# Kernel optimization log

Hardware: AMD Instinct MI355X
Metric: run time of the kernel (lower is better)

## Reference

```python
import jax, jax.numpy as jnp
import numpy as np

B, T, S, D, H, HD, DFF, NB = 2, 2048, 2048, 768, 12, 64, 3072, 32
HID = H * HD
EPS = 1e-6
NEG = -1e9


def rmsnorm(x, w):
    # T5 RMSNorm: no mean subtraction, no bias
    var = jnp.mean(jnp.square(x), axis=-1, keepdims=True)
    return x * jax.lax.rsqrt(var + EPS) * w


def sdpa(h, kv, m, wq, wk, wv, wo):
    # h: [B,Tq,D], kv: [B,Tk,D], m: additive mask broadcastable to [B,H,Tq,Tk]
    b, tq, _ = h.shape
    tk = kv.shape[1]
    q = (h @ wq).reshape(b, tq, H, HD)
    k = (kv @ wk).reshape(b, tk, H, HD)
    v = (kv @ wv).reshape(b, tk, H, HD)
    scores = jnp.einsum('bthd,bshd->bhts', q, k) + m  # scale=1.0 (T5)
    p = jax.nn.softmax(scores, axis=-1)
    y = jnp.einsum('bhts,bshd->bthd', p, v).reshape(b, tq, HID)
    return y @ wo


def setup_inputs() -> dict:
    key = jax.random.key(0)
    ks = jax.random.split(key, 16)
    x = jax.random.normal(ks[0], (B, T, D), dtype=jnp.float32)
    # causal additive mask for decoder self-attention
    causal = jnp.tril(jnp.ones((T, T), dtype=bool))
    mask = jnp.broadcast_to(jnp.where(causal, 0.0, NEG)[None, None], (B, 1, T, T)).astype(jnp.float32)
    relative_position = jax.random.randint(ks[1], (1, 1, T, T), 0, NB)
    encoder_hidden_states = jax.random.normal(ks[2], (B, S, D), dtype=jnp.float32)
    encoder_attention_mask = jnp.zeros((B, 1, T, S), dtype=jnp.float32)
    sc = 0.02
    p = {
        'sn_w': jnp.ones((D,), jnp.float32),
        'wq': sc * jax.random.normal(ks[3], (D, HID)),
        'wk': sc * jax.random.normal(ks[4], (D, HID)),
        'wv': sc * jax.random.normal(ks[5], (D, HID)),
        'wo': sc * jax.random.normal(ks[6], (HID, D)),
        'rel_emb': sc * jax.random.normal(ks[7], (NB, H)),
        'cn_w': jnp.ones((D,), jnp.float32),
        'cwq': sc * jax.random.normal(ks[8], (D, HID)),
        'cwk': sc * jax.random.normal(ks[9], (D, HID)),
        'cwv': sc * jax.random.normal(ks[10], (D, HID)),
        'cwo': sc * jax.random.normal(ks[11], (HID, D)),
        'pn_w': jnp.ones((D,), jnp.float32),
        'ffn_wi': sc * jax.random.normal(ks[12], (D, DFF)),
        'ffn_wo': sc * jax.random.normal(ks[13], (DFF, D)),
    }
    return dict(x=x, mask=mask, relative_position=relative_position,
                encoder_hidden_states=encoder_hidden_states,
                encoder_attention_mask=encoder_attention_mask, **p)


def reference(x, mask, relative_position, encoder_hidden_states, encoder_attention_mask,
              sn_w, wq, wk, wv, wo, rel_emb, cn_w, cwq, cwk, cwv, cwo, pn_w, ffn_wi, ffn_wo):
    # self-attention with relative-position bias added into additive mask
    h = rmsnorm(x, sn_w)
    # rel_emb[relative_position]: [1,1,T,T,H] -> permute(0,1,4,2,3) -> squeeze(0) -> [1,H,T,T]
    position_bias = jnp.transpose(rel_emb[relative_position], (0, 1, 4, 2, 3))[0]
    self_mask = mask + position_bias
    y = sdpa(h, h, self_mask, wq, wk, wv, wo)
    attn_out = y + x
    # cross-attention (no relative bias -> zeros position bias)
    enc_dec_position_bias = jnp.zeros_like(encoder_attention_mask)
    h2 = rmsnorm(attn_out, cn_w)
    y2 = sdpa(h2, encoder_hidden_states, encoder_attention_mask + enc_dec_position_bias,
              cwq, cwk, cwv, cwo)
    attn_out = y2 + attn_out
    # T5 FFN: relu(x @ wi) @ wo, pre-norm, residual
    hn = rmsnorm(attn_out, pn_w)
    ff = jax.nn.relu(hn @ ffn_wi) @ ffn_wo
    return (attn_out + ff, position_bias, enc_dec_position_bias)
```

## Files before the change

kernel.cpp:

```cpp
#include <hip/hip_runtime.h>
#include <hip/hip_bf16.h>
#include <stdint.h>

#define T5_B   2
#define T5_T   2048
#define T5_S   2048
#define T5_D   768
#define T5_H   12
#define T5_HD  64
#define T5_DFF 3072
#define T5_NB  32
#define NROW   4096

typedef __attribute__((ext_vector_type(8))) short bf16x8;
typedef __attribute__((ext_vector_type(4))) short short4v;
typedef __attribute__((ext_vector_type(4))) float f32x4;

__device__ __forceinline__ unsigned short f2bf(float x) {
  unsigned int u = __float_as_uint(x);
  unsigned int r = (u + 0x7FFFu + ((u >> 16) & 1u)) >> 16;
  return (unsigned short)r;
}

__device__ __forceinline__ void load_lds16(const void* g, void* l) {
  __builtin_amdgcn_global_load_lds(
      (__attribute__((address_space(1))) void*)(const_cast<void*>(g)),
      (__attribute__((address_space(3))) void*)(l), 16, 0, 0);
}

__device__ __forceinline__ unsigned cvt_pk_bf16(float lo_, float hi_) {
  unsigned d;
  asm("v_cvt_pk_bf16_f32 %0, %1, %2" : "=v"(d) : "v"(lo_), "v"(hi_));
  return d;
}

__device__ __forceinline__ f32x4 mfma16(short4v a, short4v b, f32x4 c) {
#if __has_builtin(__builtin_amdgcn_mfma_f32_16x16x16bf16_1k)
  return __builtin_amdgcn_mfma_f32_16x16x16bf16_1k(a, b, c, 0, 0, 0);
#else
  asm volatile("v_mfma_f32_16x16x16_bf16 %0, %1, %2, %0" : "+v"(c) : "v"(a), "v"(b));
  return c;
#endif
}

struct PrepArgs {
  const float* wsrc[10];
  unsigned short* wdst[10];
  const float* enc; unsigned short* encb;
  const int* rp; unsigned char* rp8;
};

__global__ __launch_bounds__(256)
void prep_kernel(PrepArgs a) {
  __shared__ float tile[32][33];
  const int bid = blockIdx.x, tid = threadIdx.x;
  if (bid < 9216) {
    int widx, rem, Kd, Nd;
    if (bid < 4608)      { widx = bid / 576; rem = bid % 576;  Kd = 768;  Nd = 768;  }
    else if (bid < 6912) { widx = 8;         rem = bid - 4608; Kd = 768;  Nd = 3072; }
    else                 { widx = 9;         rem = bid - 6912; Kd = 3072; Nd = 768;  }
    const float* W = a.wsrc[widx];
    unsigned short* Wt = a.wdst[widx];
    int nb = Nd / 32;
    int n0 = (rem % nb) * 32, k0 = (rem / nb) * 32;
    int tx = tid & 31, ty = tid >> 5;
#pragma unroll
    for (int i = 0; i < 32; i += 8)
      tile[ty + i][tx] = W[(size_t)(k0 + ty + i) * Nd + n0 + tx];
    __syncthreads();
#pragma unroll
    for (int i = 0; i < 32; i += 8)
      Wt[(size_t)(n0 + ty + i) * Kd + k0 + tx] = f2bf(tile[tx][ty + i]);
  } else if (bid < 12288) {
    int i = (bid - 9216) * 256 + tid;
    float4 v = ((const float4*)a.enc)[i];
    unsigned long long pk = (unsigned long long)f2bf(v.x)
                          | ((unsigned long long)f2bf(v.y) << 16)
                          | ((unsigned long long)f2bf(v.z) << 32)
                          | ((unsigned long long)f2bf(v.w) << 48);
    *(unsigned long long*)(a.encb + (size_t)i * 4) = pk;
  } else {
    int idx = (bid - 12288) * 256 + tid;
    const int4* src = (const int4*)(a.rp + (size_t)idx * 16);
    int4 v0 = src[0], v1 = src[1], v2 = src[2], v3 = src[3];
    uint4 o;
    o.x = (v0.x & 31) | ((v0.y & 31) << 8) | ((v0.z & 31) << 16) | ((v0.w & 31) << 24);
    o.y = (v1.x & 31) | ((v1.y & 31) << 8) | ((v1.z & 31) << 16) | ((v1.w & 31) << 24);
    o.z = (v2.x & 31) | ((v2.y & 31) << 8) | ((v2.z & 31) << 16) | ((v2.w & 31) << 24);
    o.w = (v3.x & 31) | ((v3.y & 31) << 8) | ((v3.z & 31) << 16) | ((v3.w & 31) << 24);
    ((uint4*)a.rp8)[idx] = o;
  }
}

__global__ __launch_bounds__(256)
void rmsnorm_kernel(const float* __restrict__ in, const float* __restrict__ w,
                    unsigned short* __restrict__ out) {
  int row = blockIdx.x, tid = threadIdx.x;
  const float* r = in + (size_t)row * 768;
  float x0 = r[tid], x1 = r[tid + 256], x2 = r[tid + 512];
  float s = x0 * x0 + x1 * x1 + x2 * x2;
#pragma unroll
  for (int off = 32; off > 0; off >>= 1) s += __shfl_xor(s, off);
  __shared__ float ws_[4];
  int lane = tid & 63, wv = tid >> 6;
  if (lane == 0) ws_[wv] = s;
  __syncthreads();
  float tot = ws_[0] + ws_[1] + ws_[2] + ws_[3];
  float rinv = rsqrtf(tot * (1.0f / 768.0f) + 1e-6f);
  unsigned short* o = out + (size_t)row * 768;
  o[tid]       = f2bf(x0 * rinv * w[tid]);
  o[tid + 256] = f2bf(x1 * rinv * w[tid + 256]);
  o[tid + 512] = f2bf(x2 * rinv * w[tid + 512]);
}

__global__ __launch_bounds__(256)
void pos_bias_kernel(const int* __restrict__ rp, const float* __restrict__ rel_emb,
                     float* __restrict__ out1, float* __restrict__ out2) {
  __shared__ float rl[384];
  int tid = threadIdx.x;
  for (int i = tid; i < 384; i += 256) rl[i] = rel_emb[i];
  __syncthreads();
  int t = blockIdx.y;
  int s = blockIdx.x * 1024 + tid * 4;
  int4 nb = *(const int4*)(rp + (size_t)t * 2048 + s);
#pragma unroll
  for (int h = 0; h < 12; ++h) {
    float4 v = make_float4(rl[nb.x * 12 + h], rl[nb.y * 12 + h],
                           rl[nb.z * 12 + h], rl[nb.w * 12 + h]);
    *(float4*)(out1 + ((size_t)h * 2048 + t) * 2048 + s) = v;
  }
  size_t base = (((size_t)blockIdx.y * 2 + blockIdx.x) * 256 + tid) * 8;
  float4 z = make_float4(0.f, 0.f, 0.f, 0.f);
  *(float4*)(out2 + base)     = z;
  *(float4*)(out2 + base + 4) = z;
}

__global__ __launch_bounds__(256)
void transpose_v_kernel(const unsigned short* __restrict__ vin, int stride,
                        unsigned short* __restrict__ vT) {
  __shared__ __align__(16) unsigned short tile[64][72];
  int t0 = blockIdx.x * 64, h = blockIdx.y, b = blockIdx.z;
  int tid = threadIdx.x;
  {
    int tl = tid >> 2, d0 = (tid & 3) * 16;
    const unsigned short* src = vin + (size_t)(b * 2048 + t0 + tl) * stride + h * 64 + d0;
    *(bf16x8*)&tile[tl][d0]     = *(const bf16x8*)src;
    *(bf16x8*)&tile[tl][d0 + 8] = *(const bf16x8*)(src + 8);
  }
  __syncthreads();
  {
    int d = tid >> 2, t1 = (tid & 3) * 16;
    unsigned short tmp[16] __attribute__((aligned(16)));
#pragma unroll
    for (int j = 0; j < 16; ++j) tmp[j] = tile[t1 + j][d];
    unsigned short* dst = vT + ((size_t)((b * 12 + h) * 64 + d)) * 2048 + t0 + t1;
    *(bf16x8*)dst       = *(bf16x8*)&tmp[0];
    *(bf16x8*)(dst + 8) = *(bf16x8*)&tmp[8];
  }
}

template <int TM, int TN, int EPI>
__global__ __launch_bounds__(256)
void gemm_bt(const unsigned short* __restrict__ A, const unsigned short* __restrict__ Bt,
             void* __restrict__ C, const float* __restrict__ res, int N, int K) {
  constexpr int WR = (TM >= 128) ? 2 : 1;
  constexpr int WC = 4 / WR;
  constexpr int AM = TM / WR / 16;
  constexpr int AN = TN / WC / 16;
  constexpr int CHA = TM / 8, CHB = TN / 8, CPW = (CHA + CHB) / 4;
  __shared__ __align__(16) unsigned short Als[2][TM * 64];
  __shared__ __align__(16) unsigned short Bls[2][TN * 64];
  const int tid = threadIdx.x, lane = tid & 63, wv = tid >> 6;
  const int lo = lane & 15, hi = lane >> 4;
  const int wr = wv / WC, wc = wv % WC;

  int gx = gridDim.x;
  int nwg = gx * gridDim.y;
  int f = blockIdx.y * gx + blockIdx.x;
  int q8 = nwg >> 3, r8 = nwg & 7, xcd = f & 7, base = f >> 3;
  int wg = (xcd < r8 ? xcd * (q8 + 1) : r8 * (q8 + 1) + (xcd - r8) * q8) + base;
  const int m0 = (wg / gx) * TM, n0 = (wg % gx) * TN;

  f32x4 acc[AM][AN];
#pragma unroll
  for (int i = 0; i < AM; ++i)
#pragma unroll
    for (int j = 0; j < AN; ++j) acc[i][j] = f32x4{0.f, 0.f, 0.f, 0.f};

  const int srr  = lane >> 3;
  const int scol = ((lane & 7) ^ srr) * 8;

  auto stage = [&](int k0, int bsel) {
#pragma unroll
    for (int j = 0; j < CPW; ++j) {
      int c = wv * CPW + j;
      if (c < CHA)
        load_lds16(A + (size_t)(m0 + c * 8 + srr) * K + k0 + scol, &Als[bsel][c * 512]);
      else {
        int c2 = c - CHA;
        load_lds16(Bt + (size_t)(n0 + c2 * 8 + srr) * K + k0 + scol, &Bls[bsel][c2 * 512]);
      }
    }
  };

  stage(0, 0);
  const int nIt = K >> 6;
  for (int it = 0; it < nIt; ++it) {
    const int bsel = it & 1;
    if (it + 1 < nIt) {
      stage((it + 1) << 6, bsel ^ 1);
      asm volatile("s_waitcnt vmcnt(%0)" :: "n"(CPW) : "memory");
    } else {
      asm volatile("s_waitcnt vmcnt(0)" ::: "memory");
    }
    __builtin_amdgcn_s_barrier();
    __builtin_amdgcn_sched_barrier(0);
#pragma unroll
    for (int kk = 0; kk < 2; ++kk) {
      bf16x8 af[AM], bfr[AN];
#pragma unroll
      for (int i = 0; i < AM; ++i) {
        int row = wr * (AM * 16) + i * 16 + lo;
        unsigned by = (unsigned)(row * 128) + ((unsigned)(((kk * 4 + hi) ^ (row & 7))) << 4);
        af[i] = *(const bf16x8*)((const char*)&Als[bsel][0] + by);
      }
#pragma unroll
      for (int j = 0; j < AN; ++j) {
        int row = wc * (AN * 16) + j * 16 + lo;
        unsigned by = (unsigned)(row * 128) + ((unsigned)(((kk * 4 + hi) ^ (row & 7))) << 4);
        bfr[j] = *(const bf16x8*)((const char*)&Bls[bsel][0] + by);
      }
      __builtin_amdgcn_s_setprio(1);
#pragma unroll
      for (int i = 0; i < AM; ++i)
#pragma unroll
        for (int j = 0; j < AN; ++j)
          acc[i][j] = __builtin_amdgcn_mfma_f32_16x16x32_bf16(af[i], bfr[j], acc[i][j], 0, 0, 0);
      __builtin_amdgcn_s_setprio(0);
    }
    __builtin_amdgcn_sched_barrier(0);
    __builtin_amdgcn_s_barrier();
  }

#pragma unroll
  for (int mi = 0; mi < AM; ++mi)
#pragma unroll
    for (int ni = 0; ni < AN; ++ni) {
      int row = m0 + wr * (AM * 16) + mi * 16 + hi * 4;
      int col = n0 + wc * (AN * 16) + ni * 16 + lo;
#pragma unroll
      for (int r = 0; r < 4; ++r) {
        float v = acc[mi][ni][r];
        size_t idx = (size_t)(row + r) * N + col;
        if (EPI == 0) {
          ((unsigned short*)C)[idx] = f2bf(v);
        } else if (EPI == 1) {
          ((float*)C)[idx] = v + res[idx];
        } else {
          ((unsigned short*)C)[idx] = f2bf(fmaxf(v, 0.0f));
        }
      }
    }
}

template <bool SELF>
__global__ __launch_bounds__(256)
void attn_kernel(const unsigned short* __restrict__ qp, int qstride,
                 const unsigned short* __restrict__ kp, int kstride,
                 const unsigned short* __restrict__ vT,
                 const unsigned char* __restrict__ rp8, const float* __restrict__ rel_emb,
                 unsigned short* __restrict__ yp) {
  __shared__ __align__(16) unsigned short Kls[2][4096];
  __shared__ __align__(16) unsigned short Vls[2][4096];
  __shared__ __align__(16) unsigned char rp8t[SELF ? 2 * 8192 : 16];
  __shared__ float rel_l[32];

  const int tid = threadIdx.x, lane = tid & 63, wv = tid >> 6;
  const int lo = lane & 15, hi = lane >> 4;
  const int h = blockIdx.y, b = blockIdx.z;
  const int qta = SELF ? (int)blockIdx.x : (int)blockIdx.x * 2;
  const int qtb = SELF ? 31 - (int)blockIdx.x : (int)blockIdx.x * 2 + 1;
  const int ntiles = SELF ? qtb + 1 : 32;

  if (SELF && tid < 32) rel_l[tid] = rel_emb[tid * 12 + h];

  const int qA = qta * 64 + wv * 16 + lo;
  const int qB = qtb * 64 + wv * 16 + lo;
  const unsigned short* qrA = qp + (size_t)(b * T5_T + qA) * qstride + h * 64 + hi * 8;
  const unsigned short* qrB = qp + (size_t)(b * T5_T + qB) * qstride + h * 64 + hi * 8;
  const bf16x8 qa0 = *(const bf16x8*)qrA;
  const bf16x8 qa1 = *(const bf16x8*)(qrA + 32);
  const bf16x8 qb0 = *(const bf16x8*)qrB;
  const bf16x8 qb1 = *(const bf16x8*)(qrB + 32);

  f32x4 OA[4], OB[4];
  float mA = -3.0e38f, lA = 0.f, mB = -3.0e38f, lB = 0.f;
#pragma unroll
  for (int i = 0; i < 4; ++i) { OA[i] = f32x4{0.f, 0.f, 0.f, 0.f}; OB[i] = f32x4{0.f, 0.f, 0.f, 0.f}; }

  const int krr = lane >> 3;
  const int kd0 = ((lane & 7) ^ krr) * 8;

  auto stage = [&](int kt, int bsel) {
    const int s0 = kt * 64;
#pragma unroll
    for (int j = 0; j < 2; ++j) {
      int c = wv * 2 + j;
      int rr = c * 8 + krr;
      load_lds16(kp + (size_t)(b * 2048 + s0 + rr) * kstride + h * 64 + kd0, &Kls[bsel][c * 512]);
      load_lds16(vT + (size_t)((b * 12 + h) * 64 + rr) * 2048 + s0 + kd0,    &Vls[bsel][c * 512]);
    }
    if (SELF) {
      load_lds16(rp8 + (size_t)(qtb * 64 + wv * 16 + (lane >> 2)) * 2048 + s0 + (lane & 3) * 16,
                 &rp8t[bsel * 8192 + 4096 + wv * 1024]);
      if (kt <= qta)
        load_lds16(rp8 + (size_t)(qta * 64 + wv * 16 + (lane >> 2)) * 2048 + s0 + (lane & 3) * 16,
                   &rp8t[bsel * 8192 + wv * 1024]);
    }
  };

  auto qcomp = [&](const bf16x8& qf0, const bf16x8& qf1, f32x4* Oc, float& m_, float& l_,
                   const unsigned char* rt, int qrow, bool edge, int s0,
                   const unsigned short* Kb, const unsigned short* Vb) {
    f32x4 S[4];
    __builtin_amdgcn_s_setprio(1);
#pragma unroll
    for (int ct = 0; ct < 4; ++ct) {
      int krow = ct * 16 + lo;
      unsigned by0 = ((unsigned)(krow * 128 + hi * 16))      ^ ((unsigned)(krow & 7) << 4);
      unsigned by1 = ((unsigned)(krow * 128 + 64 + hi * 16)) ^ ((unsigned)(krow & 7) << 4);
      bf16x8 kf0 = *(const bf16x8*)((const char*)Kb + by0);
      bf16x8 kf1 = *(const bf16x8*)((const char*)Kb + by1);
      f32x4 sa = f32x4{0.f, 0.f, 0.f, 0.f};
      sa = __builtin_amdgcn_mfma_f32_16x16x32_bf16(kf0, qf0, sa, 0, 0, 0);
      sa = __builtin_amdgcn_mfma_f32_16x16x32_bf16(kf1, qf1, sa, 0, 0, 0);
      S[ct] = sa;
    }
    __builtin_amdgcn_s_setprio(0);

    if (SELF) {
#pragma unroll
      for (int ct = 0; ct < 4; ++ct) {
        unsigned nb4 = *(const unsigned*)&rt[lo * 64 + ct * 16 + hi * 4];
#pragma unroll
        for (int r = 0; r < 4; ++r) {
          int s = s0 + ct * 16 + hi * 4 + r;
          float sc = S[ct][r] + rel_l[(nb4 >> (8 * r)) & 31u];
          if (edge && s > qrow) sc = -1e30f;
          S[ct][r] = sc;
        }
      }
    }

    float tm = S[0][0];
#pragma unroll
    for (int ct = 0; ct < 4; ++ct)
#pragma unroll
      for (int r = 0; r < 4; ++r) tm = fmaxf(tm, S[ct][r]);
    tm = fmaxf(tm, __shfl_xor(tm, 16));
    tm = fmaxf(tm, __shfl_xor(tm, 32));
    float mn = fmaxf(m_, tm);
    float alpha = __expf(m_ - mn);
    float rs = 0.f;
#pragma unroll
    for (int ct = 0; ct < 4; ++ct)
#pragma unroll
      for (int r = 0; r < 4; ++r) { float e = __expf(S[ct][r] - mn); S[ct][r] = e; rs += e; }
    rs += __shfl_xor(rs, 16);
    rs += __shfl_xor(rs, 32);
    l_ = l_ * alpha + rs;
    m_ = mn;
#pragma unroll
    for (int dt = 0; dt < 4; ++dt)
#pragma unroll
      for (int r = 0; r < 4; ++r) Oc[dt][r] *= alpha;

    short4v pf[4];
#pragma unroll
    for (int ct = 0; ct < 4; ++ct) {
      union { unsigned u[2]; short4v s; } cv;
      cv.u[0] = cvt_pk_bf16(S[ct][0], S[ct][1]);
      cv.u[1] = cvt_pk_bf16(S[ct][2], S[ct][3]);
      pf[ct] = cv.s;
    }

    __builtin_amdgcn_s_setprio(1);
#pragma unroll
    for (int dt = 0; dt < 4; ++dt) {
      int vrow = dt * 16 + lo;
#pragma unroll
      for (int ct = 0; ct < 4; ++ct) {
        unsigned vb = ((unsigned)(vrow * 128 + ct * 32 + hi * 8)) ^ ((unsigned)(vrow & 7) << 4);
        short4v vf = *(const short4v*)((const char*)Vb + vb);
        Oc[dt] = mfma16(vf, pf[ct], Oc[dt]);
      }
    }
    __builtin_amdgcn_s_setprio(0);
  };

  stage(0, 0);

  for (int kt = 0; kt < ntiles; ++kt) {
    const int bsel = kt & 1;
    const int s0 = kt * 64;
    asm volatile("s_waitcnt vmcnt(0)" ::: "memory");
    __syncthreads();
    if (kt + 1 < ntiles) stage(kt + 1, bsel ^ 1);

    const unsigned short* Kb = &Kls[bsel][0];
    const unsigned short* Vb = &Vls[bsel][0];

    if (!SELF || kt <= qta)
      qcomp(qa0, qa1, OA, mA, lA, &rp8t[bsel * 8192 + wv * 1024], qA,
            SELF && kt == qta, s0, Kb, Vb);
    qcomp(qb0, qb1, OB, mB, lB, &rp8t[bsel * 8192 + 4096 + wv * 1024], qB,
          SELF && kt == qtb, s0, Kb, Vb);
  }

#if !__has_builtin(__builtin_amdgcn_mfma_f32_16x16x16bf16_1k)
  asm volatile("s_nop 7\n\ts_nop 7" ::: );
#endif

  {
    float inv = 1.0f / lA;
    unsigned short* yr = yp + (size_t)(b * T5_T + qA) * 768 + h * 64 + hi * 4;
#pragma unroll
    for (int dt = 0; dt < 4; ++dt) {
      unsigned long long pk = (unsigned long long)f2bf(OA[dt][0] * inv)
                            | ((unsigned long long)f2bf(OA[dt][1] * inv) << 16)
                            | ((unsigned long long)f2bf(OA[dt][2] * inv) << 32)
                            | ((unsigned long long)f2bf(OA[dt][3] * inv) << 48);
      *(unsigned long long*)(yr + dt * 16) = pk;
    }
  }
  {
    float inv = 1.0f / lB;
    unsigned short* yr = yp + (size_t)(b * T5_T + qB) * 768 + h * 64 + hi * 4;
#pragma unroll
    for (int dt = 0; dt < 4; ++dt) {
      unsigned long long pk = (unsigned long long)f2bf(OB[dt][0] * inv)
                            | ((unsigned long long)f2bf(OB[dt][1] * inv) << 16)
                            | ((unsigned long long)f2bf(OB[dt][2] * inv) << 32)
                            | ((unsigned long long)f2bf(OB[dt][3] * inv) << 48);
      *(unsigned long long*)(yr + dt * 16) = pk;
    }
  }
}

extern "C" void kernel_launch(void* const* d_in, const int* in_sizes, int n_in,
                              void* d_out, int out_size, void* d_ws, size_t ws_size,
                              hipStream_t stream) {
  (void)in_sizes; (void)n_in; (void)out_size; (void)ws_size;
  const float* x    = (const float*)d_in[0];
  const int*   rp   = (const int*)d_in[2];
  const float* enc  = (const float*)d_in[3];
  const float* sn_w = (const float*)d_in[5];
  const float* wq   = (const float*)d_in[6];
  const float* wk   = (const float*)d_in[7];
  const float* wvw  = (const float*)d_in[8];
  const float* wo   = (const float*)d_in[9];
  const float* rel  = (const float*)d_in[10];
  const float* cn_w = (const float*)d_in[11];
  const float* cwq  = (const float*)d_in[12];
  const float* cwk  = (const float*)d_in[13];
  const float* cwv  = (const float*)d_in[14];
  const float* cwo  = (const float*)d_in[15];
  const float* pn_w = (const float*)d_in[16];
  const float* wi   = (const float*)d_in[17];
  const float* wo2  = (const float*)d_in[18];

  float* out0 = (float*)d_out;
  float* out1 = out0 + (size_t)NROW * T5_D;
  float* out2 = out1 + (size_t)T5_H * T5_T * T5_T;

  char* ws = (char*)d_ws;
  size_t off = 0;
  auto alloc = [&](size_t bytes) { char* p = ws + off; off += (bytes + 255) & ~(size_t)255; return p; };
  unsigned short* wqkvT = (unsigned short*)alloc((size_t)2304 * 768 * 2);
  unsigned short* woT   = (unsigned short*)alloc((size_t)768 * 768 * 2);
  unsigned short* wckvT = (unsigned short*)alloc((size_t)1536 * 768 * 2);
  unsigned short* wcqT  = (unsigned short*)alloc((size_t)768 * 768 * 2);
  unsigned short* wcoT  = (unsigned short*)alloc((size_t)768 * 768 * 2);
  unsigned short* wiT   = (unsigned short*)alloc((size_t)3072 * 768 * 2);
  unsigned short* woT2  = (unsigned short*)alloc((size_t)768 * 3072 * 2);
  unsigned short* normb = (unsigned short*)alloc((size_t)NROW * 768 * 2);
  unsigned short* encb  = (unsigned short*)alloc((size_t)NROW * 768 * 2);
  unsigned short* ybuf  = (unsigned short*)alloc((size_t)NROW * 768 * 2);
  float*          attn  = (float*)alloc((size_t)NROW * 768 * 4);
  unsigned char*  rp8p  = (unsigned char*)alloc((size_t)2048 * 2048);
  unsigned short* big   = (unsigned short*)alloc((size_t)NROW * 3072 * 2);
  unsigned short* vT    = big + (size_t)NROW * 2304;

  dim3 blk(256);

  {
    PrepArgs pa;
    pa.wsrc[0] = wq;  pa.wdst[0] = wqkvT;
    pa.wsrc[1] = wk;  pa.wdst[1] = wqkvT + 768 * 768;
    pa.wsrc[2] = wvw; pa.wdst[2] = wqkvT + 2 * 768 * 768;
    pa.wsrc[3] = wo;  pa.wdst[3] = woT;
    pa.wsrc[4] = cwk; pa.wdst[4] = wckvT;
    pa.wsrc[5] = cwv; pa.wdst[5] = wckvT + 768 * 768;
    pa.wsrc[6] = cwq; pa.wdst[6] = wcqT;
    pa.wsrc[7] = cwo; pa.wdst[7] = wcoT;
    pa.wsrc[8] = wi;  pa.wdst[8] = wiT;
    pa.wsrc[9] = wo2; pa.wdst[9] = woT2;
    pa.enc = enc; pa.encb = encb; pa.rp = rp; pa.rp8 = rp8p;
    prep_kernel<<<13312, blk, 0, stream>>>(pa);
  }

  rmsnorm_kernel<<<NROW, blk, 0, stream>>>(x, sn_w, normb);

  gemm_bt<128, 128, 0><<<dim3(18, 32), blk, 0, stream>>>(normb, wqkvT, big, nullptr, 2304, 768);
  transpose_v_kernel<<<dim3(32, 12, 2), blk, 0, stream>>>(big + 1536, 2304, vT);
  attn_kernel<true><<<dim3(16, 12, 2), blk, 0, stream>>>(big, 2304, big + 768, 2304, vT, rp8p, rel, ybuf);
  gemm_bt<64, 128, 1><<<dim3(6, 64), blk, 0, stream>>>(ybuf, woT, attn, x, 768, 768);

  pos_bias_kernel<<<dim3(2, 2048), blk, 0, stream>>>(rp, rel, out1, out2);

  rmsnorm_kernel<<<NROW, blk, 0, stream>>>(attn, cn_w, normb);
  gemm_bt<128, 128, 0><<<dim3(12, 32), blk, 0, stream>>>(encb, wckvT, big + (size_t)NROW * 768, nullptr, 1536, 768);
  gemm_bt<64, 128, 0><<<dim3(6, 64), blk, 0, stream>>>(normb, wcqT, big, nullptr, 768, 768);
  transpose_v_kernel<<<dim3(32, 12, 2), blk, 0, stream>>>(big + (size_t)NROW * 768 + 768, 1536, vT);
  attn_kernel<false><<<dim3(16, 12, 2), blk, 0, stream>>>(big, 768, big + (size_t)NROW * 768, 1536, vT,
                                                          nullptr, nullptr, ybuf);
  gemm_bt<64, 128, 1><<<dim3(6, 64), blk, 0, stream>>>(ybuf, wcoT, attn, attn, 768, 768);

  rmsnorm_kernel<<<NROW, blk, 0, stream>>>(attn, pn_w, normb);
  gemm_bt<128, 128, 2><<<dim3(24, 32), blk, 0, stream>>>(normb, wiT, big, nullptr, 3072, 768);
  gemm_bt<64, 128, 1><<<dim3(6, 64), blk, 0, stream>>>(big, woT2, out0, attn, 768, 3072);
}
```

Measured before the change: 386.9 us.

## Merge independent launches into fused stage kernels and split attention kernels

Folds the first RMSNorm into the prep kernel. A new stage1 kernel runs the self-QKV GEMM, the cross-KV GEMM and the position-bias output writes in a single launch, and both V transposes now share one launch. Attention is split into dedicated self and cross kernels, with smaller 64-row query tiles and XCD swizzling on the cross path. Output-projection GEMMs move to 64x64 tiles for more workgroups. The aim is fewer launches and better CU fill, at the cost of mixing heterogeneous work in one grid and extra workspace buffers.

```diff
diff --git a/kernel.cpp b/kernel.cpp
--- a/kernel.cpp
+++ b/kernel.cpp
@@ -43,16 +43,135 @@
 #endif
 }
 
+__device__ __forceinline__ int xcd_swz(int f, int nwg) {
+  int q8 = nwg >> 3, r8 = nwg & 7, xcd = f & 7, base = f >> 3;
+  return (xcd < r8 ? xcd * (q8 + 1) : r8 * (q8 + 1) + (xcd - r8) * q8) + base;
+}
+
+template <int TM, int TN, int EPI>
+__device__ __forceinline__ void gemm_body(
+    int f, int gx, int nwg,
+    const unsigned short* __restrict__ A, const unsigned short* __restrict__ Bt,
+    void* __restrict__ C, const float* __restrict__ res, int N, int K,
+    unsigned short* LDS) {
+  constexpr int WR = (TM >= 128) ? 2 : 1;
+  constexpr int WC = 4 / WR;
+  constexpr int AM = TM / WR / 16;
+  constexpr int AN = TN / WC / 16;
+  constexpr int CHA = TM / 8, CHB = TN / 8, CPW = (CHA + CHB) / 4;
+  constexpr int BUFSH = (TM + TN) * 64;
+  const int tid = threadIdx.x, lane = tid & 63, wv = tid >> 6;
+  const int lo = lane & 15, hi = lane >> 4;
+  const int wr = wv / WC, wc = wv % WC;
+  const int wg = xcd_swz(f, nwg);
+  const int m0 = (wg / gx) * TM, n0 = (wg % gx) * TN;
+
+  f32x4 acc[AM][AN];
+#pragma unroll
+  for (int i = 0; i < AM; ++i)
+#pragma unroll
+    for (int j = 0; j < AN; ++j) acc[i][j] = f32x4{0.f, 0.f, 0.f, 0.f};
+
+  const int srr  = lane >> 3;
+  const int scol = ((lane & 7) ^ srr) * 8;
+
+  auto stage = [&](int k0, int bsel) {
+    unsigned short* Ab = LDS + bsel * BUFSH;
+    unsigned short* Bb = Ab + TM * 64;
+#pragma unroll
+    for (int j = 0; j < CPW; ++j) {
+      int c = wv * CPW + j;
+      if (c < CHA)
+        load_lds16(A + (size_t)(m0 + c * 8 + srr) * K + k0 + scol, Ab + c * 512);
+      else {
+        int c2 = c - CHA;
+        load_lds16(Bt + (size_t)(n0 + c2 * 8 + srr) * K + k0 + scol, Bb + c2 * 512);
+      }
+    }
+  };
+
+  stage(0, 0);
+  const int nIt = K >> 6;
+  for (int it = 0; it < nIt; ++it) {
+    const int bsel = it & 1;
+    if (it + 1 < nIt) {
+      stage((it + 1) << 6, bsel ^ 1);
+      asm volatile("s_waitcnt vmcnt(%0)" :: "n"(CPW) : "memory");
+    } else {
+      asm volatile("s_waitcnt vmcnt(0)" ::: "memory");
+    }
+    __builtin_amdgcn_s_barrier();
+    __builtin_amdgcn_sched_barrier(0);
+    const unsigned short* Ab = LDS + bsel * BUFSH;
+    const unsigned short* Bb = Ab + TM * 64;
+#pragma unroll
+    for (int kk = 0; kk < 2; ++kk) {
+      bf16x8 af[AM], bfr[AN];
+#pragma unroll
+      for (int i = 0; i < AM; ++i) {
+        int row = wr * (AM * 16) + i * 16 + lo;
+        unsigned by = (unsigned)(row * 128) + ((unsigned)(((kk * 4 + hi) ^ (row & 7))) << 4);
+        af[i] = *(const bf16x8*)((const char*)Ab + by);
+      }
+#pragma unroll
+      for (int j = 0; j < AN; ++j) {
+        int row = wc * (AN * 16) + j * 16 + lo;
+        unsigned by = (unsigned)(row * 128) + ((unsigned)(((kk * 4 + hi) ^ (row & 7))) << 4);
+        bfr[j] = *(const bf16x8*)((const char*)Bb + by);
+      }
+      __builtin_amdgcn_s_setprio(1);
+#pragma unroll
+      for (int i = 0; i < AM; ++i)
+#pragma unroll
+        for (int j = 0; j < AN; ++j)
+          acc[i][j] = __builtin_amdgcn_mfma_f32_16x16x32_bf16(af[i], bfr[j], acc[i][j], 0, 0, 0);
+      __builtin_amdgcn_s_setprio(0);
+    }
+    __builtin_amdgcn_sched_barrier(0);
+    __builtin_amdgcn_s_barrier();
+  }
+
+#pragma unroll
+  for (int mi = 0; mi < AM; ++mi)
+#pragma unroll
+    for (int ni = 0; ni < AN; ++ni) {
+      int row = m0 + wr * (AM * 16) + mi * 16 + hi * 4;
+      int col = n0 + wc * (AN * 16) + ni * 16 + lo;
+#pragma unroll
+      for (int r = 0; r < 4; ++r) {
+        float v = acc[mi][ni][r];
+        size_t idx = (size_t)(row + r) * N + col;
+        if (EPI == 0) {
+          ((unsigned short*)C)[idx] = f2bf(v);
+        } else if (EPI == 1) {
+          ((float*)C)[idx] = v + res[idx];
+        } else {
+          ((unsigned short*)C)[idx] = f2bf(fmaxf(v, 0.0f));
+        }
+      }
+    }
+}
+
+template <int TM, int TN, int EPI>
+__global__ __launch_bounds__(256)
+void gemm_bt(const unsigned short* __restrict__ A, const unsigned short* __restrict__ Bt,
+             void* __restrict__ C, const float* __restrict__ res, int N, int K) {
+  __shared__ __align__(16) unsigned short LDS[2 * (TM + TN) * 64];
+  int f = blockIdx.y * gridDim.x + blockIdx.x;
+  gemm_body<TM, TN, EPI>(f, gridDim.x, gridDim.x * gridDim.y, A, Bt, C, res, N, K, LDS);
+}
+
 struct PrepArgs {
   const float* wsrc[10];
   unsigned short* wdst[10];
   const float* enc; unsigned short* encb;
   const int* rp; unsigned char* rp8;
+  const float* x; const float* snw; unsigned short* normb;
 };
 
 __global__ __launch_bounds__(256)
 void prep_kernel(PrepArgs a) {
-  __shared__ float tile[32][33];
+  __shared__ __align__(16) float tile[32][33];
   const int bid = blockIdx.x, tid = threadIdx.x;
   if (bid < 9216) {
     int widx, rem, Kd, Nd;
@@ -79,7 +198,7 @@
                           | ((unsigned long long)f2bf(v.z) << 32)
                           | ((unsigned long long)f2bf(v.w) << 48);
     *(unsigned long long*)(a.encb + (size_t)i * 4) = pk;
-  } else {
+  } else if (bid < 13312) {
     int idx = (bid - 12288) * 256 + tid;
     const int4* src = (const int4*)(a.rp + (size_t)idx * 16);
     int4 v0 = src[0], v1 = src[1], v2 = src[2], v3 = src[3];
@@ -89,6 +208,23 @@
     o.z = (v2.x & 31) | ((v2.y & 31) << 8) | ((v2.z & 31) << 16) | ((v2.w & 31) << 24);
     o.w = (v3.x & 31) | ((v3.y & 31) << 8) | ((v3.z & 31) << 16) | ((v3.w & 31) << 24);
     ((uint4*)a.rp8)[idx] = o;
+  } else {
+    int row = bid - 13312;
+    const float* r = a.x + (size_t)row * 768;
+    float x0 = r[tid], x1 = r[tid + 256], x2 = r[tid + 512];
+    float s = x0 * x0 + x1 * x1 + x2 * x2;
+#pragma unroll
+    for (int off = 32; off > 0; off >>= 1) s += __shfl_xor(s, off);
+    float* wsm = &tile[0][0];
+    int lane = tid & 63, wvv = tid >> 6;
+    if (lane == 0) wsm[wvv] = s;
+    __syncthreads();
+    float tot = wsm[0] + wsm[1] + wsm[2] + wsm[3];
+    float rinv = rsqrtf(tot * (1.0f / 768.0f) + 1e-6f);
+    unsigned short* o = a.normb + (size_t)row * 768;
+    o[tid]       = f2bf(x0 * rinv * a.snw[tid]);
+    o[tid + 256] = f2bf(x1 * rinv * a.snw[tid + 256]);
+    o[tid + 512] = f2bf(x2 * rinv * a.snw[tid + 512]);
   }
 }
 
@@ -113,33 +249,53 @@
   o[tid + 512] = f2bf(x2 * rinv * w[tid + 512]);
 }
 
+struct Stage1Args {
+  const unsigned short *normb, *wqkvT, *encb, *wckvT;
+  unsigned short *qkv, *ckv;
+  const int* rp; const float* rel;
+  float *out1, *out2;
+};
+
 __global__ __launch_bounds__(256)
-void pos_bias_kernel(const int* __restrict__ rp, const float* __restrict__ rel_emb,
-                     float* __restrict__ out1, float* __restrict__ out2) {
-  __shared__ float rl[384];
-  int tid = threadIdx.x;
-  for (int i = tid; i < 384; i += 256) rl[i] = rel_emb[i];
-  __syncthreads();
-  int t = blockIdx.y;
-  int s = blockIdx.x * 1024 + tid * 4;
-  int4 nb = *(const int4*)(rp + (size_t)t * 2048 + s);
-#pragma unroll
-  for (int h = 0; h < 12; ++h) {
-    float4 v = make_float4(rl[nb.x * 12 + h], rl[nb.y * 12 + h],
-                           rl[nb.z * 12 + h], rl[nb.w * 12 + h]);
-    *(float4*)(out1 + ((size_t)h * 2048 + t) * 2048 + s) = v;
-  }
-  size_t base = (((size_t)blockIdx.y * 2 + blockIdx.x) * 256 + tid) * 8;
-  float4 z = make_float4(0.f, 0.f, 0.f, 0.f);
-  *(float4*)(out2 + base)     = z;
-  *(float4*)(out2 + base + 4) = z;
+void stage1_kernel(Stage1Args a) {
+  __shared__ __align__(16) unsigned short LDS[32768];
+  const int bid = blockIdx.x, tid = threadIdx.x;
+  if (bid < 576) {
+    gemm_body<128, 128, 0>(bid, 18, 576, a.normb, a.wqkvT, a.qkv, nullptr, 2304, 768, LDS);
+  } else if (bid < 960) {
+    gemm_body<128, 128, 0>(bid - 576, 12, 384, a.encb, a.wckvT, a.ckv, nullptr, 1536, 768, LDS);
+  } else {
+    const int p = bid - 960;
+    float* rl = (float*)LDS;
+    for (int i = tid; i < 384; i += 256) rl[i] = a.rel[i];
+    __syncthreads();
+    int t = p >> 1;
+    int s = (p & 1) * 1024 + tid * 4;
+    int4 nb = *(const int4*)(a.rp + (size_t)t * 2048 + s);
+#pragma unroll
+    for (int h = 0; h < 12; ++h) {
+      float4 v = make_float4(rl[nb.x * 12 + h], rl[nb.y * 12 + h],
+                             rl[nb.z * 12 + h], rl[nb.w * 12 + h]);
+      *(float4*)(a.out1 + ((size_t)h * 2048 + t) * 2048 + s) = v;
+    }
+    size_t zbase = ((size_t)p * 256 + tid) * 8;
+    float4 z = make_float4(0.f, 0.f, 0.f, 0.f);
+    *(float4*)(a.out2 + zbase)     = z;
+    *(float4*)(a.out2 + zbase + 4) = z;
+  }
 }
 
 __global__ __launch_bounds__(256)
-void transpose_v_kernel(const unsigned short* __restrict__ vin, int stride,
-                        unsigned short* __restrict__ vT) {
+void transpose_both_kernel(const unsigned short* __restrict__ v1,
+                           const unsigned short* __restrict__ v2,
+                           unsigned short* __restrict__ vT1,
+                           unsigned short* __restrict__ vT2) {
   __shared__ __align__(16) unsigned short tile[64][72];
-  int t0 = blockIdx.x * 64, h = blockIdx.y, b = blockIdx.z;
+  int which = blockIdx.z >> 1, b = blockIdx.z & 1;
+  const unsigned short* vin = which ? v2 : v1;
+  int stride = which ? 1536 : 2304;
+  unsigned short* vT = which ? vT2 : vT1;
+  int t0 = blockIdx.x * 64, h = blockIdx.y;
   int tid = threadIdx.x;
   {
     int tl = tid >> 2, d0 = (tid & 3) * 16;
@@ -159,135 +315,126 @@
   }
 }
 
-template <int TM, int TN, int EPI>
+template <bool SELF>
+__device__ __forceinline__ void attn_qcomp(
+    const bf16x8& qf0, const bf16x8& qf1, f32x4* Oc, float& m_, float& l_,
+    const unsigned char* rt, const float* rel_l, int qrow, bool edge, int s0,
+    const unsigned short* Kb, const unsigned short* Vb, int lo, int hi) {
+  f32x4 S[4];
+  __builtin_amdgcn_s_setprio(1);
+#pragma unroll
+  for (int ct = 0; ct < 4; ++ct) {
+    int krow = ct * 16 + lo;
+    unsigned by0 = ((unsigned)(krow * 128 + hi * 16))      ^ ((unsigned)(krow & 7) << 4);
+    unsigned by1 = ((unsigned)(krow * 128 + 64 + hi * 16)) ^ ((unsigned)(krow & 7) << 4);
+    bf16x8 kf0 = *(const bf16x8*)((const char*)Kb + by0);
+    bf16x8 kf1 = *(const bf16x8*)((const char*)Kb + by1);
+    f32x4 sa = f32x4{0.f, 0.f, 0.f, 0.f};
+    sa = __builtin_amdgcn_mfma_f32_16x16x32_bf16(kf0, qf0, sa, 0, 0, 0);
+    sa = __builtin_amdgcn_mfma_f32_16x16x32_bf16(kf1, qf1, sa, 0, 0, 0);
+    S[ct] = sa;
+  }
+  __builtin_amdgcn_s_setprio(0);
+
+  if constexpr (SELF) {
+#pragma unroll
+    for (int ct = 0; ct < 4; ++ct) {
+      unsigned nb4 = *(const unsigned*)&rt[lo * 64 + ct * 16 + hi * 4];
+#pragma unroll
+      for (int r = 0; r < 4; ++r) {
+        int s = s0 + ct * 16 + hi * 4 + r;
+        float sc = S[ct][r] + rel_l[(nb4 >> (8 * r)) & 31u];
+        if (edge && s > qrow) sc = -1e30f;
+        S[ct][r] = sc;
+      }
+    }
+  }
+
+  float tm = S[0][0];
+#pragma unroll
+  for (int ct = 0; ct < 4; ++ct)
+#pragma unroll
+    for (int r = 0; r < 4; ++r) tm = fmaxf(tm, S[ct][r]);
+  tm = fmaxf(tm, __shfl_xor(tm, 16));
+  tm = fmaxf(tm, __shfl_xor(tm, 32));
+  float mn = fmaxf(m_, tm);
+  float alpha = __expf(m_ - mn);
+  float rs = 0.f;
+#pragma unroll
+  for (int ct = 0; ct < 4; ++ct)
+#pragma unroll
+    for (int r = 0; r < 4; ++r) { float e = __expf(S[ct][r] - mn); S[ct][r] = e; rs += e; }
+  rs += __shfl_xor(rs, 16);
+  rs += __shfl_xor(rs, 32);
+  l_ = l_ * alpha + rs;
+  if (tm > m_) {
+#pragma unroll
+    for (int dt = 0; dt < 4; ++dt)
+#pragma unroll
+      for (int r = 0; r < 4; ++r) Oc[dt][r] *= alpha;
+  }
+  m_ = mn;
+
+  short4v pf[4];
+#pragma unroll
+  for (int ct = 0; ct < 4; ++ct) {
+    union { unsigned u[2]; short4v s; } cv;
+    cv.u[0] = cvt_pk_bf16(S[ct][0], S[ct][1]);
+    cv.u[1] = cvt_pk_bf16(S[ct][2], S[ct][3]);
+    pf[ct] = cv.s;
+  }
+
+  __builtin_amdgcn_s_setprio(1);
+#pragma unroll
+  for (int dt = 0; dt < 4; ++dt) {
+    int vrow = dt * 16 + lo;
+#pragma unroll
+    for (int ct = 0; ct < 4; ++ct) {
+      unsigned vb = ((unsigned)(vrow * 128 + ct * 32 + hi * 8)) ^ ((unsigned)(vrow & 7) << 4);
+      short4v vf = *(const short4v*)((const char*)Vb + vb);
+      Oc[dt] = mfma16(vf, pf[ct], Oc[dt]);
+    }
+  }
+  __builtin_amdgcn_s_setprio(0);
+}
+
+__device__ __forceinline__ void attn_store(f32x4* Oc, float l_, unsigned short* yr) {
+  float inv = 1.0f / l_;
+#pragma unroll
+  for (int dt = 0; dt < 4; ++dt) {
+    unsigned long long pk = (unsigned long long)f2bf(Oc[dt][0] * inv)
+                          | ((unsigned long long)f2bf(Oc[dt][1] * inv) << 16)
+                          | ((unsigned long long)f2bf(Oc[dt][2] * inv) << 32)
+                          | ((unsigned long long)f2bf(Oc[dt][3] * inv) << 48);
+    *(unsigned long long*)(yr + dt * 16) = pk;
+  }
+}
+
 __global__ __launch_bounds__(256)
-void gemm_bt(const unsigned short* __restrict__ A, const unsigned short* __restrict__ Bt,
-             void* __restrict__ C, const float* __restrict__ res, int N, int K) {
-  constexpr int WR = (TM >= 128) ? 2 : 1;
-  constexpr int WC = 4 / WR;
-  constexpr int AM = TM / WR / 16;
-  constexpr int AN = TN / WC / 16;
-  constexpr int CHA = TM / 8, CHB = TN / 8, CPW = (CHA + CHB) / 4;
-  __shared__ __align__(16) unsigned short Als[2][TM * 64];
-  __shared__ __align__(16) unsigned short Bls[2][TN * 64];
+void attn_self_kernel(const unsigned short* __restrict__ qp,
+                      const unsigned short* __restrict__ kp,
+                      const unsigned short* __restrict__ vT,
+                      const unsigned char* __restrict__ rp8,
+                      const float* __restrict__ rel_emb,
+                      unsigned short* __restrict__ yp) {
+  __shared__ __align__(16) unsigned short Kls[2][4096];
+  __shared__ __align__(16) unsigned short Vls[2][4096];
+  __shared__ __align__(16) unsigned char rp8t[2][8192];
+  __shared__ float rel_l[32];
+
   const int tid = threadIdx.x, lane = tid & 63, wv = tid >> 6;
   const int lo = lane & 15, hi = lane >> 4;
-  const int wr = wv / WC, wc = wv % WC;
-
-  int gx = gridDim.x;
-  int nwg = gx * gridDim.y;
-  int f = blockIdx.y * gx + blockIdx.x;
-  int q8 = nwg >> 3, r8 = nwg & 7, xcd = f & 7, base = f >> 3;
-  int wg = (xcd < r8 ? xcd * (q8 + 1) : r8 * (q8 + 1) + (xcd - r8) * q8) + base;
-  const int m0 = (wg / gx) * TM, n0 = (wg % gx) * TN;
-
-  f32x4 acc[AM][AN];
-#pragma unroll
-  for (int i = 0; i < AM; ++i)
-#pragma unroll
-    for (int j = 0; j < AN; ++j) acc[i][j] = f32x4{0.f, 0.f, 0.f, 0.f};
-
-  const int srr  = lane >> 3;
-  const int scol = ((lane & 7) ^ srr) * 8;
-
-  auto stage = [&](int k0, int bsel) {
-#pragma unroll
-    for (int j = 0; j < CPW; ++j) {
-      int c = wv * CPW + j;
-      if (c < CHA)
-        load_lds16(A + (size_t)(m0 + c * 8 + srr) * K + k0 + scol, &Als[bsel][c * 512]);
-      else {
-        int c2 = c - CHA;
-        load_lds16(Bt + (size_t)(n0 + c2 * 8 + srr) * K + k0 + scol, &Bls[bsel][c2 * 512]);
-      }
-    }
-  };
-
-  stage(0, 0);
-  const int nIt = K >> 6;
-  for (int it = 0; it < nIt; ++it) {
-    const int bsel = it & 1;
-    if (it + 1 < nIt) {
-      stage((it + 1) << 6, bsel ^ 1);
-      asm volatile("s_waitcnt vmcnt(%0)" :: "n"(CPW) : "memory");
-    } else {
-      asm volatile("s_waitcnt vmcnt(0)" ::: "memory");
-    }
-    __builtin_amdgcn_s_barrier();
-    __builtin_amdgcn_sched_barrier(0);
-#pragma unroll
-    for (int kk = 0; kk < 2; ++kk) {
-      bf16x8 af[AM], bfr[AN];
-#pragma unroll
-      for (int i = 0; i < AM; ++i) {
-        int row = wr * (AM * 16) + i * 16 + lo;
-        unsigned by = (unsigned)(row * 128) + ((unsigned)(((kk * 4 + hi) ^ (row & 7))) << 4);
-        af[i] = *(const bf16x8*)((const char*)&Als[bsel][0] + by);
-      }
-#pragma unroll
-      for (int j = 0; j < AN; ++j) {
-        int row = wc * (AN * 16) + j * 16 + lo;
-        unsigned by = (unsigned)(row * 128) + ((unsigned)(((kk * 4 + hi) ^ (row & 7))) << 4);
-        bfr[j] = *(const bf16x8*)((const char*)&Bls[bsel][0] + by);
-      }
-      __builtin_amdgcn_s_setprio(1);
-#pragma unroll
-      for (int i = 0; i < AM; ++i)
-#pragma unroll
-        for (int j = 0; j < AN; ++j)
-          acc[i][j] = __builtin_amdgcn_mfma_f32_16x16x32_bf16(af[i], bfr[j], acc[i][j], 0, 0, 0);
-      __builtin_amdgcn_s_setprio(0);
-    }
-    __builtin_amdgcn_sched_barrier(0);
-    __builtin_amdgcn_s_barrier();
-  }
-
-#pragma unroll
-  for (int mi = 0; mi < AM; ++mi)
-#pragma unroll
-    for (int ni = 0; ni < AN; ++ni) {
-      int row = m0 + wr * (AM * 16) + mi * 16 + hi * 4;
-      int col = n0 + wc * (AN * 16) + ni * 16 + lo;
-#pragma unroll
-      for (int r = 0; r < 4; ++r) {
-        float v = acc[mi][ni][r];
-        size_t idx = (size_t)(row + r) * N + col;
-        if (EPI == 0) {
-          ((unsigned short*)C)[idx] = f2bf(v);
-        } else if (EPI == 1) {
-          ((float*)C)[idx] = v + res[idx];
-        } else {
-          ((unsigned short*)C)[idx] = f2bf(fmaxf(v, 0.0f));
-        }
-      }
-    }
-}
-
-template <bool SELF>
-__global__ __launch_bounds__(256)
-void attn_kernel(const unsigned short* __restrict__ qp, int qstride,
-                 const unsigned short* __restrict__ kp, int kstride,
-                 const unsigned short* __restrict__ vT,
-                 const unsigned char* __restrict__ rp8, const float* __restrict__ rel_emb,
-                 unsigned short* __restrict__ yp) {
-  __shared__ __align__(16) unsigned short Kls[2][4096];
-  __shared__ __align__(16) unsigned short Vls[2][4096];
-  __shared__ __align__(16) unsigned char rp8t[SELF ? 2 * 8192 : 16];
-  __shared__ float rel_l[32];
-
-  const int tid = threadIdx.x, lane = tid & 63, wv = tid >> 6;
-  const int lo = lane & 15, hi = lane >> 4;
-  const int h = blockIdx.y, b = blockIdx.z;
-  const int qta = SELF ? (int)blockIdx.x : (int)blockIdx.x * 2;
-  const int qtb = SELF ? 31 - (int)blockIdx.x : (int)blockIdx.x * 2 + 1;
-  const int ntiles = SELF ? qtb + 1 : 32;
-
-  if (SELF && tid < 32) rel_l[tid] = rel_emb[tid * 12 + h];
+  const int wg = xcd_swz(blockIdx.x + 16 * (blockIdx.y + 12 * blockIdx.z), 384);
+  const int xq = wg & 15, h = (wg >> 4) % 12, b = (wg >> 4) / 12;
+  const int qta = xq, qtb = 31 - xq;
+  const int ntiles = qtb + 1;
+
+  if (tid < 32) rel_l[tid] = rel_emb[tid * 12 + h];
 
   const int qA = qta * 64 + wv * 16 + lo;
   const int qB = qtb * 64 + wv * 16 + lo;
-  const unsigned short* qrA = qp + (size_t)(b * T5_T + qA) * qstride + h * 64 + hi * 8;
-  const unsigned short* qrB = qp + (size_t)(b * T5_T + qB) * qstride + h * 64 + hi * 8;
+  const unsigned short* qrA = qp + (size_t)(b * T5_T + qA) * 2304 + h * 64 + hi * 8;
+  const unsigned short* qrB = qp + (size_t)(b * T5_T + qB) * 2304 + h * 64 + hi * 8;
   const bf16x8 qa0 = *(const bf16x8*)qrA;
   const bf16x8 qa1 = *(const bf16x8*)(qrA + 32);
   const bf16x8 qb0 = *(const bf16x8*)qrB;
@@ -307,95 +454,14 @@
     for (int j = 0; j < 2; ++j) {
       int c = wv * 2 + j;
       int rr = c * 8 + krr;
-      load_lds16(kp + (size_t)(b * 2048 + s0 + rr) * kstride + h * 64 + kd0, &Kls[bsel][c * 512]);
-      load_lds16(vT + (size_t)((b * 12 + h) * 64 + rr) * 2048 + s0 + kd0,    &Vls[bsel][c * 512]);
-    }
-    if (SELF) {
-      load_lds16(rp8 + (size_t)(qtb * 64 + wv * 16 + (lane >> 2)) * 2048 + s0 + (lane & 3) * 16,
-                 &rp8t[bsel * 8192 + 4096 + wv * 1024]);
-      if (kt <= qta)
-        load_lds16(rp8 + (size_t)(qta * 64 + wv * 16 + (lane >> 2)) * 2048 + s0 + (lane & 3) * 16,
-                   &rp8t[bsel * 8192 + wv * 1024]);
-    }
-  };
-
-  auto qcomp = [&](const bf16x8& qf0, const bf16x8& qf1, f32x4* Oc, float& m_, float& l_,
-                   const unsigned char* rt, int qrow, bool edge, int s0,
-                   const unsigned short* Kb, const unsigned short* Vb) {
-    f32x4 S[4];
-    __builtin_amdgcn_s_setprio(1);
-#pragma unroll
-    for (int ct = 0; ct < 4; ++ct) {
-      int krow = ct * 16 + lo;
-      unsigned by0 = ((unsigned)(krow * 128 + hi * 16))      ^ ((unsigned)(krow & 7) << 4);
-      unsigned by1 = ((unsigned)(krow * 128 + 64 + hi * 16)) ^ ((unsigned)(krow & 7) << 4);
-      bf16x8 kf0 = *(const bf16x8*)((const char*)Kb + by0);
-      bf16x8 kf1 = *(const bf16x8*)((const char*)Kb + by1);
-      f32x4 sa = f32x4{0.f, 0.f, 0.f, 0.f};
-      sa = __builtin_amdgcn_mfma_f32_16x16x32_bf16(kf0, qf0, sa, 0, 0, 0);
-      sa = __builtin_amdgcn_mfma_f32_16x16x32_bf16(kf1, qf1, sa, 0, 0, 0);
-      S[ct] = sa;
-    }
-    __builtin_amdgcn_s_setprio(0);
-
-    if (SELF) {
-#pragma unroll
-      for (int ct = 0; ct < 4; ++ct) {
-        unsigned nb4 = *(const unsigned*)&rt[lo * 64 + ct * 16 + hi * 4];
-#pragma unroll
-        for (int r = 0; r < 4; ++r) {
-          int s = s0 + ct * 16 + hi * 4 + r;
-          float sc = S[ct][r] + rel_l[(nb4 >> (8 * r)) & 31u];
-          if (edge && s > qrow) sc = -1e30f;
-          S[ct][r] = sc;
-        }
-      }
-    }
-
-    float tm = S[0][0];
-#pragma unroll
-    for (int ct = 0; ct < 4; ++ct)
-#pragma unroll
-      for (int r = 0; r < 4; ++r) tm = fmaxf(tm, S[ct][r]);
-    tm = fmaxf(tm, __shfl_xor(tm, 16));
-    tm = fmaxf(tm, __shfl_xor(tm, 32));
-    float mn = fmaxf(m_, tm);
-    float alpha = __expf(m_ - mn);
-    float rs = 0.f;
-#pragma unroll
-    for (int ct = 0; ct < 4; ++ct)
-#pragma unroll
-      for (int r = 0; r < 4; ++r) { float e = __expf(S[ct][r] - mn); S[ct][r] = e; rs += e; }
-    rs += __shfl_xor(rs, 16);
-    rs += __shfl_xor(rs, 32);
-    l_ = l_ * alpha + rs;
-    m_ = mn;
-#pragma unroll
-    for (int dt = 0; dt < 4; ++dt)
-#pragma unroll
-      for (int r = 0; r < 4; ++r) Oc[dt][r] *= alpha;
-
-    short4v pf[4];
-#pragma unroll
-    for (int ct = 0; ct < 4; ++ct) {
-      union { unsigned u[2]; short4v s; } cv;
-      cv.u[0] = cvt_pk_bf16(S[ct][0], S[ct][1]);
-      cv.u[1] = cvt_pk_bf16(S[ct][2], S[ct][3]);
-      pf[ct] = cv.s;
-    }
-
-    __builtin_amdgcn_s_setprio(1);
-#pragma unroll
-    for (int dt = 0; dt < 4; ++dt) {
-      int vrow = dt * 16 + lo;
-#pragma unroll
-      for (int ct = 0; ct < 4; ++ct) {
-        unsigned vb = ((unsigned)(vrow * 128 + ct * 32 + hi * 8)) ^ ((unsigned)(vrow & 7) << 4);
-        short4v vf = *(const short4v*)((const char*)Vb + vb);
-        Oc[dt] = mfma16(vf, pf[ct], Oc[dt]);
-      }
-    }
-    __builtin_amdgcn_s_setprio(0);
+      load_lds16(kp + (size_t)(b * 2048 + s0 + rr) * 2304 + h * 64 + kd0, &Kls[bsel][c * 512]);
+      load_lds16(vT + (size_t)((b * 12 + h) * 64 + rr) * 2048 + s0 + kd0,  &Vls[bsel][c * 512]);
+    }
+    load_lds16(rp8 + (size_t)(qtb * 64 + wv * 16 + (lane >> 2)) * 2048 + s0 + (lane & 3) * 16,
+               &rp8t[bsel][4096 + wv * 1024]);
+    if (kt <= qta)
+      load_lds16(rp8 + (size_t)(qta * 64 + wv * 16 + (lane >> 2)) * 2048 + s0 + (lane & 3) * 16,
+                 &rp8t[bsel][wv * 1024]);
   };
 
   stage(0, 0);
@@ -410,41 +476,74 @@
     const unsigned short* Kb = &Kls[bsel][0];
     const unsigned short* Vb = &Vls[bsel][0];
 
-    if (!SELF || kt <= qta)
-      qcomp(qa0, qa1, OA, mA, lA, &rp8t[bsel * 8192 + wv * 1024], qA,
-            SELF && kt == qta, s0, Kb, Vb);
-    qcomp(qb0, qb1, OB, mB, lB, &rp8t[bsel * 8192 + 4096 + wv * 1024], qB,
-          SELF && kt == qtb, s0, Kb, Vb);
+    if (kt <= qta)
+      attn_qcomp<true>(qa0, qa1, OA, mA, lA, &rp8t[bsel][wv * 1024], rel_l, qA,
+                       kt == qta, s0, Kb, Vb, lo, hi);
+    attn_qcomp<true>(qb0, qb1, OB, mB, lB, &rp8t[bsel][4096 + wv * 1024], rel_l, qB,
+                     kt == qtb, s0, Kb, Vb, lo, hi);
   }
 
 #if !__has_builtin(__builtin_amdgcn_mfma_f32_16x16x16bf16_1k)
   asm volatile("s_nop 7\n\ts_nop 7" ::: );
 #endif
 
-  {
-    float inv = 1.0f / lA;
-    unsigned short* yr = yp + (size_t)(b * T5_T + qA) * 768 + h * 64 + hi * 4;
-#pragma unroll
-    for (int dt = 0; dt < 4; ++dt) {
-      unsigned long long pk = (unsigned long long)f2bf(OA[dt][0] * inv)
-                            | ((unsigned long long)f2bf(OA[dt][1] * inv) << 16)
-                            | ((unsigned long long)f2bf(OA[dt][2] * inv) << 32)
-                            | ((unsigned long long)f2bf(OA[dt][3] * inv) << 48);
-      *(unsigned long long*)(yr + dt * 16) = pk;
-    }
-  }
-  {
-    float inv = 1.0f / lB;
-    unsigned short* yr = yp + (size_t)(b * T5_T + qB) * 768 + h * 64 + hi * 4;
-#pragma unroll
-    for (int dt = 0; dt < 4; ++dt) {
-      unsigned long long pk = (unsigned long long)f2bf(OB[dt][0] * inv)
-                            | ((unsigned long long)f2bf(OB[dt][1] * inv) << 16)
-                            | ((unsigned long long)f2bf(OB[dt][2] * inv) << 32)
-                            | ((unsigned long long)f2bf(OB[dt][3] * inv) << 48);
-      *(unsigned long long*)(yr + dt * 16) = pk;
-    }
-  }
+  attn_store(OA, lA, yp + (size_t)(b * T5_T + qA) * 768 + h * 64 + hi * 4);
+  attn_store(OB, lB, yp + (size_t)(b * T5_T + qB) * 768 + h * 64 + hi * 4);
+}
+
+__global__ __launch_bounds__(256)
+void attn_cross_kernel(const unsigned short* __restrict__ qp,
+                       const unsigned short* __restrict__ kp,
+                       const unsigned short* __restrict__ vT,
+                       unsigned short* __restrict__ yp) {
+  __shared__ __align__(16) unsigned short Kls[2][4096];
+  __shared__ __align__(16) unsigned short Vls[2][4096];
+
+  const int tid = threadIdx.x, lane = tid & 63, wv = tid >> 6;
+  const int lo = lane & 15, hi = lane >> 4;
+  const int wg = xcd_swz(blockIdx.x + 32 * (blockIdx.y + 12 * blockIdx.z), 768);
+  const int xq = wg & 31, h = (wg >> 5) % 12, b = (wg >> 5) / 12;
+
+  const int q = xq * 64 + wv * 16 + lo;
+  const unsigned short* qr = qp + (size_t)(b * T5_T + q) * 768 + h * 64 + hi * 8;
+  const bf16x8 qf0 = *(const bf16x8*)qr;
+  const bf16x8 qf1 = *(const bf16x8*)(qr + 32);
+
+  f32x4 Oc[4];
+  float m_ = -3.0e38f, l_ = 0.f;
+#pragma unroll
+  for (int i = 0; i < 4; ++i) Oc[i] = f32x4{0.f, 0.f, 0.f, 0.f};
+
+  const int krr = lane >> 3;
+  const int kd0 = ((lane & 7) ^ krr) * 8;
+
+  auto stage = [&](int kt, int bsel) {
+    const int s0 = kt * 64;
+#pragma unroll
+    for (int j = 0; j < 2; ++j) {
+      int c = wv * 2 + j;
+      int rr = c * 8 + krr;
+      load_lds16(kp + (size_t)(b * 2048 + s0 + rr) * 1536 + h * 64 + kd0, &Kls[bsel][c * 512]);
+      load_lds16(vT + (size_t)((b * 12 + h) * 64 + rr) * 2048 + s0 + kd0, &Vls[bsel][c * 512]);
+    }
+  };
+
+  stage(0, 0);
+
+  for (int kt = 0; kt < 32; ++kt) {
+    const int bsel = kt & 1;
+    asm volatile("s_waitcnt vmcnt(0)" ::: "memory");
+    __syncthreads();
+    if (kt + 1 < 32) stage(kt + 1, bsel ^ 1);
+    attn_qcomp<false>(qf0, qf1, Oc, m_, l_, nullptr, nullptr, 0, false, kt * 64,
+                      &Kls[bsel][0], &Vls[bsel][0], lo, hi);
+  }
+
+#if !__has_builtin(__builtin_amdgcn_mfma_f32_16x16x16bf16_1k)
+  asm volatile("s_nop 7\n\ts_nop 7" ::: );
+#endif
+
+  attn_store(Oc, l_, yp + (size_t)(b * T5_T + q) * 768 + h * 64 + hi * 4);
 }
 
 extern "C" void kernel_launch(void* const* d_in, const int* in_sizes, int n_in,
@@ -486,10 +585,14 @@
   unsigned short* normb = (unsigned short*)alloc((size_t)NROW * 768 * 2);
   unsigned short* encb  = (unsigned short*)alloc((size_t)NROW * 768 * 2);
   unsigned short* ybuf  = (unsigned short*)alloc((size_t)NROW * 768 * 2);
+  unsigned short* cq    = (unsigned short*)alloc((size_t)NROW * 768 * 2);
   float*          attn  = (float*)alloc((size_t)NROW * 768 * 4);
   unsigned char*  rp8p  = (unsigned char*)alloc((size_t)2048 * 2048);
-  unsigned short* big   = (unsigned short*)alloc((size_t)NROW * 3072 * 2);
-  unsigned short* vT    = big + (size_t)NROW * 2304;
+  unsigned short* qkv   = (unsigned short*)alloc((size_t)NROW * 2304 * 2);
+  unsigned short* ckv   = (unsigned short*)alloc((size_t)NROW * 1536 * 2);
+  unsigned short* vT1   = (unsigned short*)alloc((size_t)24 * 64 * 2048 * 2);
+  unsigned short* vT2   = (unsigned short*)alloc((size_t)24 * 64 * 2048 * 2);
+  unsigned short* ffh   = (unsigned short*)alloc((size_t)NROW * 3072 * 2);
 
   dim3 blk(256);
 
@@ -506,27 +609,29 @@
     pa.wsrc[8] = wi;  pa.wdst[8] = wiT;
     pa.wsrc[9] = wo2; pa.wdst[9] = woT2;
     pa.enc = enc; pa.encb = encb; pa.rp = rp; pa.rp8 = rp8p;
-    prep_kernel<<<13312, blk, 0, stream>>>(pa);
-  }
-
-  rmsnorm_kernel<<<NROW, blk, 0, stream>>>(x, sn_w, normb);
-
-  gemm_bt<128, 128, 0><<<dim3(18, 32), blk, 0, stream>>>(normb, wqkvT, big, nullptr, 2304, 768);
-  transpose_v_kernel<<<dim3(32, 12, 2), blk, 0, stream>>>(big + 1536, 2304, vT);
-  attn_kernel<true><<<dim3(16, 12, 2), blk, 0, stream>>>(big, 2304, big + 768, 2304, vT, rp8p, rel, ybuf);
-  gemm_bt<64, 128, 1><<<dim3(6, 64), blk, 0, stream>>>(ybuf, woT, attn, x, 768, 768);
-
-  pos_bias_kernel<<<dim3(2, 2048), blk, 0, stream>>>(rp, rel, out1, out2);
+    pa.x = x; pa.snw = sn_w; pa.normb = normb;
+    prep_kernel<<<17408, blk, 0, stream>>>(pa);
+  }
+
+  {
+    Stage1Args sa;
+    sa.normb = normb; sa.wqkvT = wqkvT; sa.encb = encb; sa.wckvT = wckvT;
+    sa.qkv = qkv; sa.ckv = ckv; sa.rp = rp; sa.rel = rel;
+    sa.out1 = out1; sa.out2 = out2;
+    stage1_kernel<<<5056, blk, 0, stream>>>(sa);
+  }
+
+  transpose_both_kernel<<<dim3(32, 12, 4), blk, 0, stream>>>(qkv + 1536, ckv + 768, vT1, vT2);
+
+  attn_self_kernel<<<dim3(16, 12, 2), blk, 0, stream>>>(qkv, qkv + 768, vT1, rp8p, rel, ybuf);
+  gemm_bt<64, 64, 1><<<dim3(12, 64), blk, 0, stream>>>(ybuf, woT, attn, x, 768, 768);
 
   rmsnorm_kernel<<<NROW, blk, 0, stream>>>(attn, cn_w, normb);
-  gemm_bt<128, 128, 0><<<dim3(12, 32), blk, 0, stream>>>(encb, wckvT, big + (size_t)NROW * 768, nullptr, 1536, 768);
-  gemm_bt<64, 128, 0><<<dim3(6, 64), blk, 0, stream>>>(normb, wcqT, big, nullptr, 768, 768);
-  transpose_v_kernel<<<dim3(32, 12, 2), blk, 0, stream>>>(big + (size_t)NROW * 768 + 768, 1536, vT);
-  attn_kernel<false><<<dim3(16, 12, 2), blk, 0, stream>>>(big, 768, big + (size_t)NROW * 768, 1536, vT,
-                                                          nullptr, nullptr, ybuf);
-  gemm_bt<64, 128, 1><<<dim3(6, 64), blk, 0, stream>>>(ybuf, wcoT, attn, attn, 768, 768);
+  gemm_bt<64, 64, 0><<<dim3(12, 64), blk, 0, stream>>>(normb, wcqT, cq, nullptr, 768, 768);
+  attn_cross_kernel<<<dim3(32, 12, 2), blk, 0, stream>>>(cq, ckv, vT2, ybuf);
+  gemm_bt<64, 64, 1><<<dim3(12, 64), blk, 0, stream>>>(ybuf, wcoT, attn, attn, 768, 768);
 
   rmsnorm_kernel<<<NROW, blk, 0, stream>>>(attn, pn_w, normb);
-  gemm_bt<128, 128, 2><<<dim3(24, 32), blk, 0, stream>>>(normb, wiT, big, nullptr, 3072, 768);
-  gemm_bt<64, 128, 1><<<dim3(6, 64), blk, 0, stream>>>(big, woT2, out0, attn, 768, 3072);
-}
+  gemm_bt<128, 128, 2><<<dim3(24, 32), blk, 0, stream>>>(normb, wiT, ffh, nullptr, 3072, 768);
+  gemm_bt<64, 64, 1><<<dim3(12, 64), blk, 0, stream>>>(ffh, woT2, out0, attn, 768, 3072);
+}
```

Result: faster. 360.8 us (-6.8%).
